# Optimization experiments

Hardware: AMD Instinct MI355X
Metric: run time of the kernel (lower is better)

## Reference

```python
import jax, jax.numpy as jnp
import numpy as np

B, T, HID, OUT = 8, 256, 256, 6
DT = 0.1

def setup_inputs() -> dict:
    key = jax.random.key(0)
    ks = jax.random.split(key, 16)
    n = lambda i, shp, s: jax.random.normal(ks[i], shp, jnp.float32) * s
    return {
        "frames": jax.random.normal(ks[0], (B, T, 3, 64, 64), jnp.float32),
        "hidden_state": jnp.zeros((B, HID), jnp.float32),
        "conv1_w": n(1, (32, 3, 3, 3), 0.2), "conv1_b": jnp.zeros((32,), jnp.float32),
        "conv2_w": n(2, (64, 32, 3, 3), 0.1), "conv2_b": jnp.zeros((64,), jnp.float32),
        "conv3_w": n(3, (128, 64, 3, 3), 0.1), "conv3_b": jnp.zeros((128,), jnp.float32),
        "enc_w": n(4, (HID, 128), 0.08), "enc_b": jnp.zeros((HID,), jnp.float32),
        "ltc_wr": n(5, (HID, HID), 0.05), "ltc_wi": n(6, (HID, HID), 0.05),
        "ltc_b": jnp.zeros((HID,), jnp.float32),
        "ltc_tau": jax.random.uniform(ks[7], (HID,), jnp.float32, 0.5, 1.5),
        "ltc_a": n(8, (HID,), 1.0),
        "dec_w1": n(9, (128, HID), 0.08), "dec_b1": jnp.zeros((128,), jnp.float32),
        "dec_w2": n(10, (64, 128), 0.1), "dec_b2": jnp.zeros((64,), jnp.float32),
        "dec_w3": n(11, (OUT, 64), 0.1), "dec_b3": jnp.zeros((OUT,), jnp.float32),
    }

def _conv(x, w, b):
    y = jax.lax.conv_general_dilated(x, w, (2, 2), [(1, 1), (1, 1)],
                                     dimension_numbers=("NCHW", "OIHW", "NCHW"))
    return y + b[None, :, None, None]

def reference(frames, hidden_state, conv1_w, conv1_b, conv2_w, conv2_b, conv3_w, conv3_b,
              enc_w, enc_b, ltc_wr, ltc_wi, ltc_b, ltc_tau, ltc_a,
              dec_w1, dec_b1, dec_w2, dec_b2, dec_w3, dec_b3):
    Bb, Tt = frames.shape[:2]
    x = frames.reshape(Bb * Tt, 3, 64, 64)
    x = jax.nn.relu(_conv(x, conv1_w, conv1_b))   # (BT,32,32,32)
    x = jax.nn.relu(_conv(x, conv2_w, conv2_b))   # (BT,64,16,16)
    x = jax.nn.relu(_conv(x, conv3_w, conv3_b))   # (BT,128,8,8); adaptive pool to (8,8) is identity here
    feats = x.reshape(Bb, Tt, 128, 8, 8).transpose(0, 1, 3, 4, 2).reshape(Bb, Tt, 64, 128)
    node = feats @ enc_w.T + enc_b                # (B,T,64,HID)
    x_seq = node.mean(axis=2).transpose(1, 0, 2)  # (T,B,HID)

    def step(h, x_t):
        # LTC Euler update, dt=0.1, n_steps=1
        f = jnp.tanh(h @ ltc_wr.T + x_t @ ltc_wi.T + ltc_b)
        h_new = h + DT * (-(1.0 / ltc_tau + f) * h + f * ltc_a)
        y = jax.nn.relu(h_new @ dec_w1.T + dec_b1)
        y = jax.nn.relu(y @ dec_w2.T + dec_b2)
        c = y @ dec_w3.T + dec_b3
        return h_new, c

    final_hidden, controls = jax.lax.scan(step, hidden_state, x_seq)
    return controls.transpose(1, 0, 2), final_hidden
```

## Files before the change

kernel.cpp:

```cpp
#include <hip/hip_runtime.h>

#define T_STEPS 256
#define B_SZ 8
#define HID 256

typedef _Float16 hv2 __attribute__((ext_vector_type(2)));
typedef _Float16 f16x4 __attribute__((ext_vector_type(4)));
typedef float f32x4 __attribute__((ext_vector_type(4)));
union H2U { hv2 h; unsigned u; };
union U2F { uint2 u; f16x4 h; };
__device__ inline hv2 u2h(unsigned u){ H2U c; c.u = u; return c.h; }
__device__ inline unsigned h2u(hv2 h){ H2U c; c.h = h; return c.u; }
__device__ inline hv2 relu2(hv2 v){
  unsigned u = h2u(v);
  unsigned s = (u & 0x80008000u) >> 15;
  u &= ~(s * 0xFFFFu);
  return u2h(u);
}
__device__ inline unsigned packh2f(float lo, float hi){
  hv2 h; h.x = (_Float16)lo; h.y = (_Float16)hi; return h2u(h);
}

#define OFF_XW   0
#define OFF_HH   524288
#define OFF_WFT  1141760
#define OFF_BF   1174528
#define OFF_D1T  1174784
#define OFF_D2T  1207552
#define OFF_D3T  1215744
#define OFF_W1P  1216128
#define OFF_W2F  1216560
#define OFF_W3F  1225776
#define OFF_WRP  1262640

#define ENC_LDS_DW 16264

__global__ __launch_bounds__(256) void prep_kernel(
    const float* __restrict__ conv1_w, const float* __restrict__ conv2_w,
    const float* __restrict__ conv3_w, const float* __restrict__ enc_w,
    const float* __restrict__ enc_b,  const float* __restrict__ ltc_wi,
    const float* __restrict__ ltc_b,  const float* __restrict__ ltc_wr,
    const float* __restrict__ dec_w1,
    const float* __restrict__ dec_w2, const float* __restrict__ dec_w3,
    float* __restrict__ ws)
{
  int gtid = blockIdx.x * 256 + threadIdx.x;
  int nth = gridDim.x * 256;
  unsigned* wsu = (unsigned*)ws;
  for (int e = gtid; e < 128 * 256; e += nth) {
    int j = e >> 7, m = e & 127;
    float s = 0.f;
    for (int k = 0; k < 256; ++k) s = fmaf(ltc_wi[j*256 + k], enc_w[k*128 + m], s);
    ws[OFF_WFT + m*256 + j] = s;
  }
  for (int e = gtid; e < 256; e += nth) {
    float s = ltc_b[e];
    for (int k = 0; k < 256; ++k) s = fmaf(ltc_wi[e*256 + k], enc_b[k], s);
    ws[OFF_BF + e] = s;
  }
  for (int e = gtid; e < 27*16; e += nth) { int k = e>>4, p = e&15;
    wsu[OFF_W1P+e] = packh2f(conv1_w[(2*p)*27 + k], conv1_w[(2*p+1)*27 + k]); }
  for (int e = gtid; e < 9216; e += nth) {
    int dpair = e & 1;
    int nt = (e >> 1) & 3;
    int l  = (e >> 3) & 63;
    int g  = e >> 9;
    int kt = g % 9, hp = g / 9;
    int oc = nt*16 + (l & 15);
    int ic = hp*16 + ((l>>4)<<2) + (dpair<<1);
    int ky = kt/3, kx = kt%3;
    wsu[OFF_W2F + e] = packh2f(conv2_w[((oc*32 + ic)*3 + ky)*3 + kx],
                               conv2_w[((oc*32 + ic+1)*3 + ky)*3 + kx]);
  }
  for (int e = gtid; e < 36864; e += nth) {
    int dpair = e & 1;
    int tmp = e >> 1;
    int l = tmp & 63; tmp >>= 6;
    int nt = tmp & 7; tmp >>= 3;
    int kt = tmp;
    int kyx = kt >> 2;
    int ky = kyx/3, kx = kyx%3;
    int ic = ((kt & 3) << 4) + ((l>>4)<<2) + (dpair<<1);
    int oc = nt*16 + (l & 15);
    wsu[OFF_W3F + e] = packh2f(conv3_w[((oc*64 + ic)*3 + ky)*3 + kx],
                               conv3_w[((oc*64 + ic+1)*3 + ky)*3 + kx]);
  }
  for (int e = gtid; e < 32768; e += nth) {
    int i = e & 31;
    int j = (e >> 5) & 255;
    int q = e >> 13;
    wsu[OFF_WRP + e] = packh2f(ltc_wr[j*256 + q*64 + 2*i],
                               ltc_wr[j*256 + q*64 + 2*i + 1]);
  }
  for (int e = gtid; e < 256*128;e += nth) { int k = e>>7, i = e&127; ws[OFF_D1T+e] = dec_w1[i*256 + k]; }
  for (int e = gtid; e < 128*64; e += nth) { int k = e>>6, i = e&63;  ws[OFF_D2T+e] = dec_w2[i*128 + k]; }
  for (int e = gtid; e < 64*6;   e += nth) { int k = e/6,  o = e%6;   ws[OFF_D3T+e] = dec_w3[o*64 + k]; }
}

__global__ __launch_bounds__(256, 2) void enc_kernel(
    const float* __restrict__ frames,
    const float* __restrict__ b1, const float* __restrict__ b2,
    const float* __restrict__ b3, float* __restrict__ ws)
{
  extern __shared__ __align__(16) unsigned lds[];
  unsigned* buf0  = lds;
  unsigned* frH   = lds + 8192;
  unsigned* w3buf = lds + 8192;
  unsigned* w1s   = lds + 15320;
  float* fmp = (float*)(lds + 15752);
  _Float16* frHh = (_Float16*)frH;

  const int tid = threadIdx.x;
  const int l   = tid & 63;
  const int w   = tid >> 6;
  const int kg  = l >> 4;
  const int lc  = l & 15;
  const int bt  = blockIdx.x;
  const int b   = bt >> 8, t = bt & 255;
  const float* fr = frames + (size_t)bt * 12288;
  const unsigned* wsu = (const unsigned*)ws;
  const uint4* w2f4 = (const uint4*)(wsu + OFF_W2F);
  const uint4* w3src = (const uint4*)(wsu + OFF_W3F);

  {
    uint4 z4 = make_uint4(0u, 0u, 0u, 0u);
    for (int i = tid; i < 1782; i += 256) ((uint4*)frH)[i] = z4;
    if (tid < 216) ((uint2*)w1s)[tid] = ((const uint2*)(wsu + OFF_W1P))[tid];
  }
  __syncthreads();
  {
    const float4* fr4 = (const float4*)fr;
    #pragma unroll
    for (int p = 0; p < 12; ++p) {
      int fidx = p*256 + tid;
      float4 v = fr4[fidx];
      int ic = fidx >> 10, rem = fidx & 1023;
      int iy = rem >> 4, xq = rem & 15;
      int dw = ic*2376 + (iy+1)*36 + 2*xq + 2;
      uint2 pk;
      pk.x = packh2f(v.x, v.y);
      pk.y = packh2f(v.z, v.w);
      *(uint2*)(frH + dw) = pk;
    }
  }
  __syncthreads();

  f32x4 acc2[4][4];
  #pragma unroll
  for (int mi = 0; mi < 4; ++mi)
    #pragma unroll
    for (int nt = 0; nt < 4; ++nt) {
      float bb = b2[nt*16 + lc];
      acc2[mi][nt] = (f32x4){bb, bb, bb, bb};
    }

  for (int hp = 0; hp < 2; ++hp) {
    for (int p = 0; p < 4; ++p) {
      int pos = p*256 + tid;
      int y = pos >> 5, x = pos & 31;
      int base = 2*y*72 + 2*x;
      hv2 a1[8];
      #pragma unroll
      for (int o = 0; o < 8; ++o) { a1[o].x = (_Float16)b1[16*hp+2*o]; a1[o].y = (_Float16)b1[16*hp+2*o+1]; }
      #pragma unroll
      for (int ic = 0; ic < 3; ++ic)
        #pragma unroll
        for (int ky = 0; ky < 3; ++ky)
          #pragma unroll
          for (int kx = 0; kx < 3; ++kx) {
            _Float16 hf = frHh[base + ic*4752 + ky*72 + kx + 3];
            hv2 vs; vs.x = hf; vs.y = hf;
            int k = ic*9 + ky*3 + kx;
            uint4 wa = ((uint4*)w1s)[k*4 + hp*2];
            uint4 wb = ((uint4*)w1s)[k*4 + hp*2 + 1];
            a1[0] = vs * u2h(wa.x) + a1[0];
            a1[1] = vs * u2h(wa.y) + a1[1];
            a1[2] = vs * u2h(wa.z) + a1[2];
            a1[3] = vs * u2h(wa.w) + a1[3];
            a1[4] = vs * u2h(wb.x) + a1[4];
            a1[5] = vs * u2h(wb.y) + a1[5];
            a1[6] = vs * u2h(wb.z) + a1[6];
            a1[7] = vs * u2h(wb.w) + a1[7];
          }
      unsigned r0 = h2u(relu2(a1[0])), r1 = h2u(relu2(a1[1]));
      unsigned r2 = h2u(relu2(a1[2])), r3 = h2u(relu2(a1[3]));
      unsigned r4 = h2u(relu2(a1[4])), r5 = h2u(relu2(a1[5]));
      unsigned r6 = h2u(relu2(a1[6])), r7 = h2u(relu2(a1[7]));
      int s = pos & 3;
      uint4 v0, v1;
      if (s & 1) { v0 = make_uint4(r2,r3,r0,r1); v1 = make_uint4(r6,r7,r4,r5); }
      else       { v0 = make_uint4(r0,r1,r2,r3); v1 = make_uint4(r4,r5,r6,r7); }
      int sl = (s >> 1) & 1;
      ((uint4*)buf0)[pos*2 + sl]     = v0;
      ((uint4*)buf0)[pos*2 + (1^sl)] = v1;
    }
    __syncthreads();
    #pragma unroll
    for (int ky = 0; ky < 3; ++ky)
      #pragma unroll
      for (int kx = 0; kx < 3; ++kx) {
        int kt = ky*3 + kx;
        int bidx = ((hp*9 + kt)*64 + l)*2;
        uint4 q0 = w2f4[bidx];
        uint4 q1 = w2f4[bidx + 1];
        U2F bf[4];
        bf[0].u = make_uint2(q0.x, q0.y);
        bf[1].u = make_uint2(q0.z, q0.w);
        bf[2].u = make_uint2(q1.x, q1.y);
        bf[3].u = make_uint2(q1.z, q1.w);
        #pragma unroll
        for (int mi = 0; mi < 4; ++mi) {
          int mt = w*4 + mi;
          int iy = 2*mt - 1 + ky;
          if (iy >= 0) {
            int ix = 2*lc - 1 + kx;
            bool okx = (unsigned)ix < 32u;
            int pos1 = iy*32 + (okx ? ix : 0);
            U2F av; av.u = ((const uint2*)buf0)[pos1*4 + (kg ^ (pos1 & 3))];
            if (!okx) { av.u.x = 0u; av.u.y = 0u; }
            #pragma unroll
            for (int nt = 0; nt < 4; ++nt)
              acc2[mi][nt] = __builtin_amdgcn_mfma_f32_16x16x16f16(av.h, bf[nt].h, acc2[mi][nt], 0, 0, 0);
          }
        }
      }
    __syncthreads();
  }

  {
    uint4 s0a = w3src[tid];
    uint4 s0b = w3src[256 + tid];
    _Float16* act2h = (_Float16*)buf0;
    #pragma unroll
    for (int mi = 0; mi < 4; ++mi)
      #pragma unroll
      for (int nt = 0; nt < 4; ++nt)
        #pragma unroll
        for (int i = 0; i < 4; ++i) {
          int pos = (w*4 + mi)*16 + 4*kg + i;
          int oc = nt*16 + lc;
          float vv = fmaxf(acc2[mi][nt][i], 0.f);
          int ocp = (((oc >> 2) ^ (pos & 7)) << 2) + (oc & 3);
          act2h[pos*64 + ocp] = (_Float16)vv;
        }
    ((uint4*)w3buf)[tid] = s0a;
    ((uint4*)w3buf)[256 + tid] = s0b;
  }

  f32x4 acc3[8];
  #pragma unroll
  for (int nt = 0; nt < 8; ++nt) { float bb = b3[nt*16 + lc]; acc3[nt] = (f32x4){bb, bb, bb, bb}; }
  const int y3 = (w*16 + lc) >> 3, x3 = lc & 7;
  __syncthreads();

  for (int cc = 0; cc < 18; ++cc) {
    uint4 st0, st1;
    if (cc < 17) {
      st0 = w3src[(cc+1)*512 + tid];
      st1 = w3src[(cc+1)*512 + 256 + tid];
    }
    int kyx = cc >> 1;
    int ky = kyx / 3, kx = kyx % 3;
    int iy = 2*y3 - 1 + ky, ix = 2*x3 - 1 + kx;
    bool ok = ((unsigned)iy < 16u) && ((unsigned)ix < 16u);
    int posIn = (ok ? iy : 0)*16 + (ok ? ix : 0);
    int sw = posIn & 7;
    const uint2* bvp = (const uint2*)w3buf + (cc & 1)*1024;
    #pragma unroll
    for (int k2 = 0; k2 < 2; ++k2) {
      int kt = 2*cc + k2;
      int icb = (kt & 3)*4 + kg;
      U2F av; av.u = ((const uint2*)buf0)[posIn*16 + (icb ^ sw)];
      if (!ok) { av.u.x = 0u; av.u.y = 0u; }
      #pragma unroll
      for (int nt = 0; nt < 8; ++nt) {
        U2F bv; bv.u = bvp[((k2*8 + nt)<<6) + l];
        acc3[nt] = __builtin_amdgcn_mfma_f32_16x16x16f16(av.h, bv.h, acc3[nt], 0, 0, 0);
      }
    }
    if (cc < 17) {
      ((uint4*)w3buf)[((cc+1)&1)*512 + tid] = st0;
      ((uint4*)w3buf)[((cc+1)&1)*512 + 256 + tid] = st1;
    }
    __syncthreads();
  }

  #pragma unroll
  for (int nt = 0; nt < 8; ++nt) {
    float s = 0.f;
    #pragma unroll
    for (int i = 0; i < 4; ++i) s += fmaxf(acc3[nt][i], 0.f);
    s += __shfl_xor(s, 16);
    s += __shfl_xor(s, 32);
    if (l < 16) fmp[w*128 + nt*16 + l] = s;
  }
  __syncthreads();
  if (tid < 128) {
    float s = fmp[tid] + fmp[128 + tid] + fmp[256 + tid] + fmp[384 + tid];
    fmp[tid] = s * (1.f/64.f);
  }
  __syncthreads();
  {
    float accx = ws[OFF_BF + tid];
    const float* wfT = ws + OFF_WFT;
    for (int m = 0; m < 128; ++m) accx = fmaf(fmp[m], wfT[m*256 + tid], accx);
    ws[OFF_XW + (t*B_SZ + b)*HID + tid] = accx;
  }
}

__global__ __launch_bounds__(1024) void scan_kernel(
    const float* __restrict__ tau, const float* __restrict__ av,
    const float* __restrict__ h0,
    float* __restrict__ ws, float* __restrict__ outh)
{
  const int b = blockIdx.x;
  const int tid = threadIdx.x;
  const int j = tid & 255, q = tid >> 8;
  __shared__ float hf[256];
  __shared__ unsigned hp16[128];
  __shared__ float part[4][256];
  __shared__ float hbuf[16*256];

  uint4 wv[8];
  {
    const uint4* wp = (const uint4*)((const unsigned*)ws + OFF_WRP + (q*256 + j)*32);
    #pragma unroll
    for (int r = 0; r < 8; ++r) wv[r] = wp[r];
  }
  const float tinv = 1.f / tau[j];
  const float aj = av[j];
  const float* xw = ws + OFF_XW;
  float* hh = ws + OFF_HH;

  {
    float hv0 = h0[b*256 + j];
    float hvn = __shfl_xor(hv0, 1);
    if (q == 0) {
      hf[j] = hv0;
      if (!(j & 1)) hp16[j >> 1] = packh2f(hv0, hvn);
    }
  }
  float xw_pref = xw[(0*B_SZ + b)*HID + j];
  __syncthreads();

  for (int t = 0; t < T_STEPS; ++t) {
    float xwv = xw_pref;
    xw_pref = xw[((t+1)*B_SZ + b)*HID + j];
    hv2 acc = {(_Float16)0.f, (_Float16)0.f};
    const uint4* hq = (const uint4*)hp16 + q*8;
    #pragma unroll
    for (int r = 0; r < 8; ++r) {
      uint4 hvp = hq[r];
      acc = u2h(hvp.x) * u2h(wv[r].x) + acc;
      acc = u2h(hvp.y) * u2h(wv[r].y) + acc;
      acc = u2h(hvp.z) * u2h(wv[r].z) + acc;
      acc = u2h(hvp.w) * u2h(wv[r].w) + acc;
    }
    float hv0 = hf[j];
    part[q][j] = (float)acc.x + (float)acc.y;
    __syncthreads();
    float pre = part[0][j] + part[1][j] + part[2][j] + part[3][j] + xwv;
    float f = 1.f - 2.f / (1.f + __expf(2.f * pre));
    float hn = fmaf(0.1f, fmaf(-(tinv + f), hv0, f * aj), hv0);
    float hnn = __shfl_xor(hn, 1);
    if (q == 0) {
      hf[j] = hn;
      hbuf[(t & 15)*256 + j] = hn;
      if (!(j & 1)) hp16[j >> 1] = packh2f(hn, hnn);
    }
    __syncthreads();
    if ((t & 15) == 15) {
      int base = t - 15;
      int st = tid >> 6;
      int col = (tid & 63) << 2;
      *(float4*)(hh + ((base + st)*B_SZ + b)*HID + col) = *(float4*)(hbuf + st*256 + col);
    }
  }
  if (q == 0) outh[b*HID + j] = hf[j];
}

__global__ __launch_bounds__(256) void dec_kernel(
    const float* __restrict__ db1, const float* __restrict__ db2,
    const float* __restrict__ db3, const float* __restrict__ ws,
    float* __restrict__ outc)
{
  const int bid = blockIdx.x;
  const int b = bid >> 8, t = bid & 255;
  const int tid = threadIdx.x;
  __shared__ float hloc[256];
  __shared__ float p1[2][128];
  __shared__ float y1s[128];
  __shared__ float p2[4][64];
  __shared__ float y2s[64];
  const float* hh  = ws + OFF_HH + (t*B_SZ + b)*HID;
  const float* d1T = ws + OFF_D1T;
  const float* d2T = ws + OFF_D2T;
  const float* d3T = ws + OFF_D3T;
  hloc[tid] = hh[tid];
  __syncthreads();
  {
    int i = tid & 127, hf = tid >> 7;
    float s = 0.f;
    for (int k = hf*128; k < hf*128 + 128; ++k) s = fmaf(hloc[k], d1T[k*128 + i], s);
    p1[hf][i] = s;
  }
  __syncthreads();
  if (tid < 128) y1s[tid] = fmaxf(p1[0][tid] + p1[1][tid] + db1[tid], 0.f);
  __syncthreads();
  {
    int i = tid & 63, r = tid >> 6;
    float s = 0.f;
    for (int k = r*32; k < r*32 + 32; ++k) s = fmaf(y1s[k], d2T[k*64 + i], s);
    p2[r][i] = s;
  }
  __syncthreads();
  if (tid < 64) y2s[tid] = fmaxf(p2[0][tid] + p2[1][tid] + p2[2][tid] + p2[3][tid] + db2[tid], 0.f);
  __syncthreads();
  if (tid < 6) {
    float s = db3[tid];
    for (int k = 0; k < 64; ++k) s = fmaf(y2s[k], d3T[k*6 + tid], s);
    outc[(b*T_STEPS + t)*6 + tid] = s;
  }
}

extern "C" void kernel_launch(void* const* d_in, const int* in_sizes, int n_in,
                              void* d_out, int out_size, void* d_ws, size_t ws_size,
                              hipStream_t stream)
{
  const float* frames = (const float*)d_in[0];
  const float* h0   = (const float*)d_in[1];
  const float* c1w  = (const float*)d_in[2];
  const float* c1b  = (const float*)d_in[3];
  const float* c2w  = (const float*)d_in[4];
  const float* c2b  = (const float*)d_in[5];
  const float* c3w  = (const float*)d_in[6];
  const float* c3b  = (const float*)d_in[7];
  const float* encw = (const float*)d_in[8];
  const float* encb = (const float*)d_in[9];
  const float* wr   = (const float*)d_in[10];
  const float* wi   = (const float*)d_in[11];
  const float* lb   = (const float*)d_in[12];
  const float* ltau = (const float*)d_in[13];
  const float* la   = (const float*)d_in[14];
  const float* dw1  = (const float*)d_in[15];
  const float* db1  = (const float*)d_in[16];
  const float* dw2  = (const float*)d_in[17];
  const float* db2  = (const float*)d_in[18];
  const float* dw3  = (const float*)d_in[19];
  const float* db3  = (const float*)d_in[20];
  float* out = (float*)d_out;
  float* ws  = (float*)d_ws;

  hipLaunchKernelGGL(prep_kernel, dim3(256), dim3(256), 0, stream,
                     c1w, c2w, c3w, encw, encb, wi, lb, wr, dw1, dw2, dw3, ws);
  hipLaunchKernelGGL(enc_kernel, dim3(2048), dim3(256), ENC_LDS_DW*4, stream,
                     frames, c1b, c2b, c3b, ws);
  hipLaunchKernelGGL(scan_kernel, dim3(B_SZ), dim3(1024), 0, stream,
                     ltau, la, h0, ws, out + 12288);
  hipLaunchKernelGGL(dec_kernel, dim3(2048), dim3(256), 0, stream,
                     db1, db2, db3, ws, out);
}
```

Before: 408.5 us.

## Collapse scan kernel to 256 threads with register-held weights and double-buffered h

The LTC recurrence kernel drops from 1024 to 256 threads per block, so each thread keeps its whole row of the fp16 recurrent weights in registers (128 dwords). This removes the cross-quarter partial-sum reduction through shared memory and one of the two barriers per step. The packed hidden state is double-buffered, and the fp32 hidden value lives in a register instead of shared memory. In exchange each thread does four times the dot-product work on the serial critical path and register pressure rises, which risks spills. The x-projection prefetch is also removed.

```diff
diff --git a/kernel.cpp b/kernel.cpp
--- a/kernel.cpp
+++ b/kernel.cpp
@@ -308,75 +308,72 @@
   }
 }
 
-__global__ __launch_bounds__(1024) void scan_kernel(
+__global__ __launch_bounds__(256, 1) void scan_kernel(
     const float* __restrict__ tau, const float* __restrict__ av,
     const float* __restrict__ h0,
     float* __restrict__ ws, float* __restrict__ outh)
 {
   const int b = blockIdx.x;
-  const int tid = threadIdx.x;
-  const int j = tid & 255, q = tid >> 8;
-  __shared__ float hf[256];
-  __shared__ unsigned hp16[128];
-  __shared__ float part[4][256];
+  const int j = threadIdx.x;
+  __shared__ unsigned hp16[2][128];
   __shared__ float hbuf[16*256];
 
-  uint4 wv[8];
-  {
-    const uint4* wp = (const uint4*)((const unsigned*)ws + OFF_WRP + (q*256 + j)*32);
-    #pragma unroll
-    for (int r = 0; r < 8; ++r) wv[r] = wp[r];
+  uint4 wv[32];
+  {
+    const uint4* wp = (const uint4*)((const unsigned*)ws + OFF_WRP);
+    #pragma unroll
+    for (int q = 0; q < 4; ++q)
+      #pragma unroll
+      for (int r = 0; r < 8; ++r)
+        wv[q*8 + r] = wp[(q*256 + j)*8 + r];
   }
   const float tinv = 1.f / tau[j];
   const float aj = av[j];
   const float* xw = ws + OFF_XW;
   float* hh = ws + OFF_HH;
 
-  {
-    float hv0 = h0[b*256 + j];
-    float hvn = __shfl_xor(hv0, 1);
-    if (q == 0) {
-      hf[j] = hv0;
-      if (!(j & 1)) hp16[j >> 1] = packh2f(hv0, hvn);
-    }
-  }
-  float xw_pref = xw[(0*B_SZ + b)*HID + j];
+  float hreg = h0[b*256 + j];
+  {
+    float hnn = __shfl_xor(hreg, 1);
+    if (!(j & 1)) hp16[0][j >> 1] = packh2f(hreg, hnn);
+  }
   __syncthreads();
 
   for (int t = 0; t < T_STEPS; ++t) {
-    float xwv = xw_pref;
-    xw_pref = xw[((t+1)*B_SZ + b)*HID + j];
-    hv2 acc = {(_Float16)0.f, (_Float16)0.f};
-    const uint4* hq = (const uint4*)hp16 + q*8;
-    #pragma unroll
-    for (int r = 0; r < 8; ++r) {
-      uint4 hvp = hq[r];
-      acc = u2h(hvp.x) * u2h(wv[r].x) + acc;
-      acc = u2h(hvp.y) * u2h(wv[r].y) + acc;
-      acc = u2h(hvp.z) * u2h(wv[r].z) + acc;
-      acc = u2h(hvp.w) * u2h(wv[r].w) + acc;
-    }
-    float hv0 = hf[j];
-    part[q][j] = (float)acc.x + (float)acc.y;
-    __syncthreads();
-    float pre = part[0][j] + part[1][j] + part[2][j] + part[3][j] + xwv;
+    float xwv = xw[(t*B_SZ + b)*HID + j];
+    const uint4* hq = (const uint4*)hp16[t & 1];
+    hv2 a0 = {(_Float16)0.f, (_Float16)0.f};
+    hv2 a1 = a0, a2 = a0, a3 = a0;
+    #pragma unroll
+    for (int r = 0; r < 32; ++r) {
+      uint4 hv = hq[r];
+      uint4 wr4 = wv[r];
+      a0 = u2h(hv.x) * u2h(wr4.x) + a0;
+      a1 = u2h(hv.y) * u2h(wr4.y) + a1;
+      a2 = u2h(hv.z) * u2h(wr4.z) + a2;
+      a3 = u2h(hv.w) * u2h(wr4.w) + a3;
+    }
+    hv2 s2 = (a0 + a1) + (a2 + a3);
+    float pre = (float)s2.x + (float)s2.y + xwv;
     float f = 1.f - 2.f / (1.f + __expf(2.f * pre));
-    float hn = fmaf(0.1f, fmaf(-(tinv + f), hv0, f * aj), hv0);
+    float hn = fmaf(0.1f, fmaf(-(tinv + f), hreg, f * aj), hreg);
     float hnn = __shfl_xor(hn, 1);
-    if (q == 0) {
-      hf[j] = hn;
-      hbuf[(t & 15)*256 + j] = hn;
-      if (!(j & 1)) hp16[j >> 1] = packh2f(hn, hnn);
-    }
+    if (!(j & 1)) hp16[(t + 1) & 1][j >> 1] = packh2f(hn, hnn);
+    hbuf[(t & 15)*256 + j] = hn;
+    hreg = hn;
     __syncthreads();
     if ((t & 15) == 15) {
       int base = t - 15;
-      int st = tid >> 6;
-      int col = (tid & 63) << 2;
-      *(float4*)(hh + ((base + st)*B_SZ + b)*HID + col) = *(float4*)(hbuf + st*256 + col);
-    }
-  }
-  if (q == 0) outh[b*HID + j] = hf[j];
+      #pragma unroll
+      for (int r = 0; r < 4; ++r) {
+        int row = (j >> 6) + r*4;
+        int col = (j & 63) << 2;
+        *(float4*)(hh + ((base + row)*B_SZ + b)*HID + col) = *(float4*)(hbuf + row*256 + col);
+      }
+      __syncthreads();
+    }
+  }
+  outh[b*256 + j] = hreg;
 }
 
 __global__ __launch_bounds__(256) void dec_kernel(
@@ -455,7 +452,7 @@
                      c1w, c2w, c3w, encw, encb, wi, lb, wr, dw1, dw2, dw3, ws);
   hipLaunchKernelGGL(enc_kernel, dim3(2048), dim3(256), ENC_LDS_DW*4, stream,
                      frames, c1b, c2b, c3b, ws);
-  hipLaunchKernelGGL(scan_kernel, dim3(B_SZ), dim3(1024), 0, stream,
+  hipLaunchKernelGGL(scan_kernel, dim3(B_SZ), dim3(256), 0, stream,
                      ltau, la, h0, ws, out + 12288);
   hipLaunchKernelGGL(dec_kernel, dim3(2048), dim3(256), 0, stream,
                      db1, db2, db3, ws, out);
```

Result: slower. 431.7 us (+5.7%).
